# Kernel optimization log

Hardware: AMD Instinct MI355X
Metric: run time of the kernel (lower is better)

## Reference

```python
import jax, jax.numpy as jnp
import numpy as np

HID = 2048          # hidden_size
INTER = 4096        # expand * hidden_size
NH = 64             # num_heads
HD = 64             # head_dim (NH*HD == INTER)
N = 128             # ssm state_size
G = 1               # n_groups
K = 4               # conv_kernel
EPS = 1e-5
CONV_DIM = INTER + 2 * G * N            # 4352
PROJ = INTER + CONV_DIM + NH            # 8512 (d_mlp == 0)


def setup_inputs() -> dict:
    key = jax.random.key(0)
    ks = jax.random.split(key, 6)
    B, S = 2, 2048
    return {
        "hidden_states": jax.random.normal(ks[0], (B, S, HID), jnp.float32),
        "in_proj_w": jax.random.normal(ks[1], (PROJ, HID), jnp.float32) * 0.02,
        "conv_w": jax.random.normal(ks[2], (CONV_DIM, 1, K), jnp.float32) * 0.1,
        "conv_b": jax.random.normal(ks[3], (CONV_DIM,), jnp.float32) * 0.02,
        "dt_bias": jnp.ones((NH,), jnp.float32),
        "A_log": jnp.log(jnp.arange(1, NH + 1, dtype=jnp.float32)),
        "D": jnp.ones((NH,), jnp.float32),
        "norm_weight": jnp.ones((INTER,), jnp.float32),
        "out_proj_w": jax.random.normal(ks[4], (HID, INTER), jnp.float32) * 0.02,
    }


def _mamba2_forward(hidden_states, in_proj_w, conv_w, conv_b, dt_bias,
                    A_log, D, norm_weight, out_proj_w):
    b, sq, _ = hidden_states.shape
    # in_proj (d_mlp == 0, so split is gate | hidden_B_C | dt)
    proj = hidden_states @ in_proj_w.T                       # [b, s, PROJ]
    gate, hbc, dt = jnp.split(proj, [INTER, INTER + CONV_DIM], axis=-1)

    # causal depthwise conv1d over time + SiLU
    xc = jnp.transpose(hbc, (0, 2, 1))                       # [b, conv_dim, s]
    xc = jax.lax.conv_general_dilated(xc, conv_w, (1,), [(K - 1, 0)],
                                      feature_group_count=CONV_DIM)
    xc = xc + conv_b[None, :, None]
    hbc = jax.nn.silu(jnp.transpose(xc, (0, 2, 1)))          # [b, s, conv_dim]

    hs, Bm, Cm = jnp.split(hbc, [INTER, INTER + G * N], axis=-1)
    hs = hs.reshape(b, sq, NH, HD)
    Bm = jnp.repeat(Bm.reshape(b, sq, G, N), NH // G, axis=2)   # [b, s, nh, n]
    Cm = jnp.repeat(Cm.reshape(b, sq, G, N), NH // G, axis=2)

    A = -jnp.exp(A_log)                                      # [nh]
    dt = jax.nn.softplus(dt + dt_bias)                       # [b, s, nh]

    # selective SSM scan: state_t = exp(dt*A)*state_{t-1} + dt*B_t x_t^T
    def step(state, inp):
        xt, Bt, Ct, dtt = inp                                # [b,nh,hd],[b,nh,n],[b,nh,n],[b,nh]
        dA = jnp.exp(dtt * A)                                # [b, nh]
        state = state * dA[..., None, None] \
            + (dtt[..., None] * xt)[..., None] * Bt[:, :, None, :]
        y = jnp.einsum('bhdn,bhn->bhd', state, Ct)
        return state, y

    init = jnp.zeros((b, NH, HD, N), jnp.float32)
    xs = (jnp.moveaxis(hs, 1, 0), jnp.moveaxis(Bm, 1, 0),
          jnp.moveaxis(Cm, 1, 0), jnp.moveaxis(dt, 1, 0))
    _, ys = jax.lax.scan(step, init, xs)                     # [s, b, nh, hd]
    y = jnp.moveaxis(ys, 0, 1) + D[None, None, :, None] * hs
    y = y.reshape(b, sq, INTER)

    # gated RMSNorm (norm_before_gate=False): gate first, then normalize
    y = y * jax.nn.silu(gate)
    var = jnp.mean(y * y, axis=-1, keepdims=True)
    y = y * jax.lax.rsqrt(var + EPS) * norm_weight
    return y @ out_proj_w.T                                  # [b, s, HID]


def reference(hidden_states, in_proj_w, conv_w, conv_b, dt_bias, A_log, D,
              norm_weight, out_proj_w):
    return _mamba2_forward(hidden_states, in_proj_w, conv_w, conv_b, dt_bias,
                           A_log, D, norm_weight, out_proj_w)
```

## Files before the change

### kernel.cpp

```cpp
#include <hip/hip_runtime.h>
#include <hip/hip_bf16.h>
#include <cstddef>
#include <cstdint>

#define HID   2048
#define INTER 4096
#define NH    64
#define HD    64
#define NST   128
#define CONV_DIM 4352
#define PROJ  8512
#define PROJ_PAD 8704
#define SS    2048
#define BB    2
#define BS    (BB*SS)
#define EPS   1e-5f

#define COL_HS 4096
#define COL_B  8192
#define COL_C  8320
#define COL_DT 8448

#define NCHC  64
#define CHUNKC 32
#define CV8   (CONV_DIM / 8)

#define CL    128
#define NCHK  16

typedef short s16x8 __attribute__((ext_vector_type(8)));
typedef float f32x4 __attribute__((ext_vector_type(4)));

__device__ inline ushort f2b(float x) {
  __hip_bfloat16 h = __float2bfloat16(x);
  return *(ushort*)&h;
}
__device__ inline float b2f(ushort u) {
  unsigned int v = ((unsigned int)u) << 16;
  return __uint_as_float(v);
}
__device__ inline int swz(int row, int e) { return row * 128 + (e ^ ((row & 7) << 3)); }

__device__ inline void gload16(const void* g, void* l) {
  __builtin_amdgcn_global_load_lds((const __attribute__((address_space(1))) void*)g,
                                   (__attribute__((address_space(3))) void*)l, 16, 0, 0);
}

#define N4A  ((long)BS * HID / 4)
#define N4W1 ((long)PROJ_PAD * HID / 4)
#define N4W2 ((long)HID * INTER / 4)

__global__ __launch_bounds__(256) void convert_all(
    const float* __restrict__ hs, const float* __restrict__ w1,
    const float* __restrict__ w2, ushort* __restrict__ hs16,
    ushort* __restrict__ w1p, ushort* __restrict__ w216) {
  long i = (long)blockIdx.x * 256 + threadIdx.x;
  const float* src;
  ushort* dst;
  long e0;
  if (i < N4A) {
    src = hs; dst = hs16; e0 = i * 4;
  } else if (i < N4A + N4W1) {
    long k = i - N4A;
    e0 = k * 4;
    long row = e0 >> 11;
    if (row >= PROJ) {
      ushort4 z = {0, 0, 0, 0};
      *(ushort4*)(w1p + e0) = z;
      return;
    }
    src = w1; dst = w1p;
  } else if (i < N4A + N4W1 + N4W2) {
    long k = i - N4A - N4W1;
    src = w2; dst = w216; e0 = k * 4;
  } else {
    return;
  }
  float4 v = *(const float4*)(src + e0);
  ushort4 o;
  o.x = f2b(v.x); o.y = f2b(v.y); o.z = f2b(v.z); o.w = f2b(v.w);
  *(ushort4*)(dst + e0) = o;
}

__global__ __launch_bounds__(512, 2) void gemm256_8ph(
    const ushort* __restrict__ A, const ushort* __restrict__ Bw,
    ushort* __restrict__ C, float* __restrict__ dtbuf) {
  __shared__ ushort smem[65536];
  const int tid = threadIdx.x;
  const int lane = tid & 63;
  const int wid = tid >> 6;
  const int wm = wid >> 2;
  const int wn = wid & 3;
  const int r = lane & 15;
  const int kx = lane >> 4;

  const int fid = blockIdx.x;
  const int bcol = ((fid >> 7) << 3) + ((fid & 127) >> 4);
  const int brow = fid & 15;

  const ushort* Ag = A + (size_t)(brow * 256) * HID;
  const ushort* Bg = Bw + (size_t)(bcol * 256) * HID;

  const int srow = tid >> 3;
  const int scole = (((tid & 7) * 16) ^ ((srow & 7) << 4)) >> 1;

  auto stageA = [&](int buf, int kt, int half) {
    const ushort* g = Ag + (size_t)(half * 128 + srow) * HID + kt * 64 + scole;
    ushort* l = smem + buf * 16384 + half * 8192 + tid * 8;
    gload16(g, l);
    gload16(g + (size_t)64 * HID, l + 4096);
  };
  auto stageB = [&](int buf, int kt, int half) {
    const ushort* g = Bg + (size_t)(half * 128 + srow) * HID + kt * 64 + scole;
    ushort* l = smem + 32768 + buf * 16384 + half * 8192 + tid * 8;
    gload16(g, l);
    gload16(g + (size_t)64 * HID, l + 4096);
  };
  auto ldA = [&](int buf, int mf, int ks) -> s16x8 {
    int row = wm * 128 + mf * 16 + r;
    int cb = (ks * 64 + kx * 16) ^ ((row & 7) << 4);
    return *(const s16x8*)(smem + buf * 16384 + row * 64 + (cb >> 1));
  };
  auto ldB = [&](int buf, int nf, int ks) -> s16x8 {
    int row = wn * 64 + nf * 16 + r;
    int cb = (ks * 64 + kx * 16) ^ ((row & 7) << 4);
    return *(const s16x8*)(smem + 32768 + buf * 16384 + row * 64 + (cb >> 1));
  };

  f32x4 acc[8][4];
#pragma unroll
  for (int i = 0; i < 8; i++)
#pragma unroll
    for (int j = 0; j < 4; j++) acc[i][j] = (f32x4)0.f;

  constexpr int NT = HID / 64;

  stageA(0, 0, 0); stageA(0, 0, 1);
  stageB(0, 0, 0); stageB(0, 0, 1);
  stageA(1, 1, 0); stageA(1, 1, 1);
  asm volatile("s_waitcnt vmcnt(4)" ::: "memory");
  __builtin_amdgcn_s_barrier();

  int cur = 0;
  for (int t = 0; t < NT; t++) {
    s16x8 a[4][2], b[2][2], b2[2][2];
#pragma unroll
    for (int mf = 0; mf < 4; mf++)
#pragma unroll
      for (int ks = 0; ks < 2; ks++) a[mf][ks] = ldA(cur, mf, ks);
#pragma unroll
    for (int nf = 0; nf < 2; nf++)
#pragma unroll
      for (int ks = 0; ks < 2; ks++) b[nf][ks] = ldB(cur, nf, ks);
    if (t + 1 < NT) stageB(cur ^ 1, t + 1, 0);
    __builtin_amdgcn_s_barrier();
    asm volatile("s_waitcnt lgkmcnt(0)" ::: "memory");
    __builtin_amdgcn_sched_barrier(0);
    __builtin_amdgcn_s_setprio(1);
#pragma unroll
    for (int mf = 0; mf < 4; mf++)
#pragma unroll
      for (int nf = 0; nf < 2; nf++)
#pragma unroll
        for (int ks = 0; ks < 2; ks++)
          acc[mf][nf] = __builtin_amdgcn_mfma_f32_16x16x32_bf16(a[mf][ks], b[nf][ks], acc[mf][nf], 0, 0, 0);
    __builtin_amdgcn_s_setprio(0);
    __builtin_amdgcn_s_barrier();
#pragma unroll
    for (int nf = 0; nf < 2; nf++)
#pragma unroll
      for (int ks = 0; ks < 2; ks++) b2[nf][ks] = ldB(cur, nf + 2, ks);
    if (t + 1 < NT) stageB(cur ^ 1, t + 1, 1);
    __builtin_amdgcn_s_barrier();
    asm volatile("s_waitcnt lgkmcnt(0)" ::: "memory");
    __builtin_amdgcn_sched_barrier(0);
    __builtin_amdgcn_s_setprio(1);
#pragma unroll
    for (int mf = 0; mf < 4; mf++)
#pragma unroll
      for (int nf = 0; nf < 2; nf++)
#pragma unroll
        for (int ks = 0; ks < 2; ks++)
          acc[mf][nf + 2] = __builtin_amdgcn_mfma_f32_16x16x32_bf16(a[mf][ks], b2[nf][ks], acc[mf][nf + 2], 0, 0, 0);
    __builtin_amdgcn_s_setprio(0);
    __builtin_amdgcn_s_barrier();
#pragma unroll
    for (int mf = 0; mf < 4; mf++)
#pragma unroll
      for (int ks = 0; ks < 2; ks++) a[mf][ks] = ldA(cur, mf + 4, ks);
    __builtin_amdgcn_s_barrier();
    asm volatile("s_waitcnt lgkmcnt(0)" ::: "memory");
    __builtin_amdgcn_sched_barrier(0);
    __builtin_amdgcn_s_setprio(1);
#pragma unroll
    for (int mf = 0; mf < 4; mf++)
#pragma unroll
      for (int nf = 0; nf < 2; nf++)
#pragma unroll
        for (int ks = 0; ks < 2; ks++)
          acc[mf + 4][nf] = __builtin_amdgcn_mfma_f32_16x16x32_bf16(a[mf][ks], b[nf][ks], acc[mf + 4][nf], 0, 0, 0);
    __builtin_amdgcn_s_setprio(0);
    __builtin_amdgcn_s_barrier();
    if (t + 2 < NT) { stageA(cur, t + 2, 0); stageA(cur, t + 2, 1); }
    __builtin_amdgcn_s_setprio(1);
#pragma unroll
    for (int mf = 0; mf < 4; mf++)
#pragma unroll
      for (int nf = 0; nf < 2; nf++)
#pragma unroll
        for (int ks = 0; ks < 2; ks++)
          acc[mf + 4][nf + 2] = __builtin_amdgcn_mfma_f32_16x16x32_bf16(a[mf][ks], b2[nf][ks], acc[mf + 4][nf + 2], 0, 0, 0);
    __builtin_amdgcn_s_setprio(0);
    if (t + 2 < NT) {
      asm volatile("s_waitcnt vmcnt(4)" ::: "memory");
    } else {
      asm volatile("s_waitcnt vmcnt(0)" ::: "memory");
    }
    __builtin_amdgcn_s_barrier();
    cur ^= 1;
  }

  const int m0 = brow * 256 + wm * 128 + (lane >> 4) * 4;
  const int n0 = bcol * 256 + wn * 64 + r;
#pragma unroll
  for (int mf = 0; mf < 8; mf++) {
#pragma unroll
    for (int nf = 0; nf < 4; nf++) {
      int n = n0 + nf * 16;
      if (n >= PROJ) continue;
#pragma unroll
      for (int q = 0; q < 4; q++) {
        float v = acc[mf][nf][q];
        int m = m0 + mf * 16 + q;
        C[(size_t)m * PROJ + n] = f2b(v);
        if (n >= COL_DT) dtbuf[(size_t)m * 64 + (n - COL_DT)] = v;
      }
    }
  }
}

__global__ __launch_bounds__(512, 2) void gemm2_256x128(
    const ushort* __restrict__ A, const ushort* __restrict__ Bw,
    float* __restrict__ C) {
  __shared__ ushort smem[49152];
  const int tid = threadIdx.x;
  const int lane = tid & 63;
  const int wid = tid >> 6;
  const int wm = wid >> 1;
  const int wn = wid & 1;
  const int r = lane & 15;
  const int kx = lane >> 4;

  const int fid = blockIdx.x;
  const int bcol = fid >> 4;
  const int brow = fid & 15;

  const ushort* Ag = A + (size_t)(brow * 256) * PROJ;
  const ushort* Bg = Bw + (size_t)(bcol * 128) * INTER;

  const int srow = tid >> 3;
  const int scole = (((tid & 7) * 16) ^ ((srow & 7) << 4)) >> 1;

  auto stageA2 = [&](int buf, int kt) {
#pragma unroll
    for (int i = 0; i < 4; i++) {
      gload16(Ag + (size_t)(i * 64 + srow) * PROJ + kt * 64 + scole,
              smem + buf * 16384 + i * 4096 + tid * 8);
    }
  };
  auto stageB2 = [&](int buf, int kt) {
#pragma unroll
    for (int i = 0; i < 2; i++) {
      gload16(Bg + (size_t)(i * 64 + srow) * INTER + kt * 64 + scole,
              smem + 32768 + buf * 8192 + i * 4096 + tid * 8);
    }
  };
  auto ldA2 = [&](int buf, int mf, int ks) -> s16x8 {
    int row = wm * 64 + mf * 16 + r;
    int cb = (ks * 64 + kx * 16) ^ ((row & 7) << 4);
    return *(const s16x8*)(smem + buf * 16384 + row * 64 + (cb >> 1));
  };
  auto ldB2 = [&](int buf, int nf, int ks) -> s16x8 {
    int row = wn * 64 + nf * 16 + r;
    int cb = (ks * 64 + kx * 16) ^ ((row & 7) << 4);
    return *(const s16x8*)(smem + 32768 + buf * 8192 + row * 64 + (cb >> 1));
  };

  f32x4 acc[4][4];
#pragma unroll
  for (int i = 0; i < 4; i++)
#pragma unroll
    for (int j = 0; j < 4; j++) acc[i][j] = (f32x4)0.f;

  constexpr int NT = INTER / 64;

  stageA2(0, 0); stageB2(0, 0);
  stageA2(1, 1); stageB2(1, 1);
  asm volatile("s_waitcnt vmcnt(6)" ::: "memory");
  __builtin_amdgcn_s_barrier();

  int cur = 0;
  for (int t = 0; t < NT; t++) {
    s16x8 a[4][2], b[4][2];
#pragma unroll
    for (int mf = 0; mf < 4; mf++)
#pragma unroll
      for (int ks = 0; ks < 2; ks++) a[mf][ks] = ldA2(cur, mf, ks);
#pragma unroll
    for (int nf = 0; nf < 4; nf++)
#pragma unroll
      for (int ks = 0; ks < 2; ks++) b[nf][ks] = ldB2(cur, nf, ks);
    __builtin_amdgcn_s_barrier();
    asm volatile("s_waitcnt lgkmcnt(0)" ::: "memory");
    __builtin_amdgcn_sched_barrier(0);
    __builtin_amdgcn_s_setprio(1);
#pragma unroll
    for (int mf = 0; mf < 4; mf++)
#pragma unroll
      for (int nf = 0; nf < 2; nf++)
#pragma unroll
        for (int ks = 0; ks < 2; ks++)
          acc[mf][nf] = __builtin_amdgcn_mfma_f32_16x16x32_bf16(a[mf][ks], b[nf][ks], acc[mf][nf], 0, 0, 0);
    __builtin_amdgcn_s_setprio(0);
    __builtin_amdgcn_s_barrier();
    if (t + 2 < NT) { stageA2(cur, t + 2); stageB2(cur, t + 2); }
    __builtin_amdgcn_s_setprio(1);
#pragma unroll
    for (int mf = 0; mf < 4; mf++)
#pragma unroll
      for (int nf = 2; nf < 4; nf++)
#pragma unroll
        for (int ks = 0; ks < 2; ks++)
          acc[mf][nf] = __builtin_amdgcn_mfma_f32_16x16x32_bf16(a[mf][ks], b[nf][ks], acc[mf][nf], 0, 0, 0);
    __builtin_amdgcn_s_setprio(0);
    if (t + 2 < NT) {
      asm volatile("s_waitcnt vmcnt(6)" ::: "memory");
    } else {
      asm volatile("s_waitcnt vmcnt(0)" ::: "memory");
    }
    __builtin_amdgcn_s_barrier();
    cur ^= 1;
  }

  const int m0 = brow * 256 + wm * 64 + (lane >> 4) * 4;
  const int n0 = bcol * 128 + wn * 64 + r;
#pragma unroll
  for (int mf = 0; mf < 4; mf++) {
#pragma unroll
    for (int nf = 0; nf < 4; nf++) {
      int n = n0 + nf * 16;
#pragma unroll
      for (int q = 0; q < 4; q++)
        C[(size_t)(m0 + mf * 16 + q) * HID + n] = acc[mf][nf][q];
    }
  }
}

__global__ __launch_bounds__(256) void conv_capture(
    const ushort* __restrict__ proj, ushort* __restrict__ side) {
  int idx = blockIdx.x * 256 + threadIdx.x;
  const int total = BB * NCHC * 3 * CV8;
  if (idx >= total) return;
  int c8 = idx % CV8;
  int t = idx / CV8;
  int j = t % 3; t /= 3;
  int chunk = t % NCHC;
  int b = t / NCHC;
  int s = chunk * CHUNKC - 1 - j;
  s16x8 v = {0, 0, 0, 0, 0, 0, 0, 0};
  if (s >= 0) v = *(const s16x8*)(proj + ((size_t)b * SS + s) * PROJ + COL_HS + c8 * 8);
  *(s16x8*)(side + ((size_t)(b * NCHC + chunk) * 3 + j) * CONV_DIM + c8 * 8) = v;
}

__global__ __launch_bounds__(256) void conv_silu(
    ushort* __restrict__ proj, const ushort* __restrict__ side,
    const float* __restrict__ cw, const float* __restrict__ cb) {
  int idx = blockIdx.x * 256 + threadIdx.x;
  const int total = BB * NCHC * CV8;
  if (idx >= total) return;
  int c8 = idx % CV8;
  int t = idx / CV8;
  int chunk = t % NCHC;
  int b = t / NCHC;
  const int c0 = c8 * 8;
  float w0[8], w1[8], w2[8], w3[8], bias[8], h1[8], h2[8], h3[8];
#pragma unroll
  for (int e = 0; e < 8; e++) {
    float4 wv = *(const float4*)(cw + (c0 + e) * 4);
    w0[e] = wv.x; w1[e] = wv.y; w2[e] = wv.z; w3[e] = wv.w;
    bias[e] = cb[c0 + e];
  }
  const ushort* sd = side + (size_t)(b * NCHC + chunk) * 3 * CONV_DIM;
  {
    s16x8 v1 = *(const s16x8*)(sd + c0);
    s16x8 v2 = *(const s16x8*)(sd + CONV_DIM + c0);
    s16x8 v3 = *(const s16x8*)(sd + 2 * CONV_DIM + c0);
#pragma unroll
    for (int e = 0; e < 8; e++) {
      h1[e] = b2f((ushort)v1[e]);
      h2[e] = b2f((ushort)v2[e]);
      h3[e] = b2f((ushort)v3[e]);
    }
  }
  size_t p = ((size_t)b * SS + (size_t)chunk * CHUNKC) * PROJ + COL_HS + c0;
  for (int s = 0; s < CHUNKC; s++) {
    s16x8 xv = *(const s16x8*)(proj + p);
    s16x8 ov;
#pragma unroll
    for (int e = 0; e < 8; e++) {
      float x = b2f((ushort)xv[e]);
      float o = w3[e] * x + w2[e] * h1[e] + w1[e] * h2[e] + w0[e] * h3[e] + bias[e];
      o = o / (1.f + __expf(-o));
      ov[e] = (short)f2b(o);
      h3[e] = h2[e]; h2[e] = h1[e]; h1[e] = x;
    }
    *(s16x8*)(proj + p) = ov;
    p += PROJ;
  }
}

__global__ __launch_bounds__(256) void ssd_chunk_state(
    const ushort* __restrict__ proj, const float* __restrict__ dtf,
    const float* __restrict__ dt_bias, const float* __restrict__ A_log,
    ushort* __restrict__ states, float* __restrict__ cumbuf,
    float* __restrict__ dtvbuf) {
  const int bid = blockIdx.x;
  const int c = bid & 15;
  const int h = (bid >> 4) & 63;
  const int b = bid >> 10;
  const int tid = threadIdx.x;
  const int lane = tid & 63;
  const int wv = tid >> 6;
  __shared__ float sdtv[CL], scum[CL], sw[CL];
  __shared__ float wtot[2];
  __shared__ ushort sBt[128 * 128];
  __shared__ ushort sXw[64 * 128];
  const size_t row0 = (size_t)b * SS + (size_t)c * CL;
  const size_t bh = (size_t)(b * NH + h);

  const float Ah = -__expf(A_log[h]);
  float dtvv = 0.f, v = 0.f;
  if (tid < CL) {
    float z = dtf[(row0 + tid) * 64 + h] + dt_bias[h];
    dtvv = (z > 20.f) ? z : log1pf(__expf(z));
    v = dtvv * Ah;
  }
#pragma unroll
  for (int off = 1; off < 64; off <<= 1) {
    float u = __shfl_up(v, off);
    if (lane >= off) v += u;
  }
  if (tid < CL && lane == 63) wtot[wv] = v;
  __syncthreads();
  if (wv == 1) v += wtot[0];
  if (tid < CL) {
    sdtv[tid] = dtvv;
    scum[tid] = v;
    cumbuf[bh * SS + c * CL + tid] = v;
    dtvbuf[bh * SS + c * CL + tid] = dtvv;
  }
  __syncthreads();
  const float cumL = scum[CL - 1];
  if (tid < CL) sw[tid] = __expf(cumL - v) * dtvv;
  __syncthreads();

  {
    const int t = tid >> 1, n0 = (tid & 1) * 64;
    const ushort* src = proj + (row0 + t) * PROJ + COL_B + n0;
#pragma unroll
    for (int j = 0; j < 64; j += 8) {
      s16x8 vv = *(const s16x8*)(src + j);
#pragma unroll
      for (int e = 0; e < 8; e++) sBt[swz(n0 + j + e, t)] = (ushort)vv[e];
    }
  }
  {
    const int d = tid & 63;
    const int t0 = (tid >> 6) * 32;
    for (int t = t0; t < t0 + 32; t++) {
      float x = b2f(proj[(row0 + t) * PROJ + COL_HS + h * 64 + d]);
      sXw[swz(d, t)] = f2b(x * sw[t]);
    }
  }
  __syncthreads();

  const int r = lane & 15, kx = lane >> 4;
  f32x4 acc[2][4];
#pragma unroll
  for (int i = 0; i < 2; i++)
#pragma unroll
    for (int j = 0; j < 4; j++) acc[i][j] = (f32x4)0.f;
#pragma unroll
  for (int kk = 0; kk < 4; kk++) {
    s16x8 a[2], bo[4];
#pragma unroll
    for (int i = 0; i < 2; i++)
      a[i] = *(const s16x8*)&sBt[swz(wv * 32 + i * 16 + r, kk * 32 + kx * 8)];
#pragma unroll
    for (int j = 0; j < 4; j++)
      bo[j] = *(const s16x8*)&sXw[swz(j * 16 + r, kk * 32 + kx * 8)];
#pragma unroll
    for (int i = 0; i < 2; i++)
#pragma unroll
      for (int j = 0; j < 4; j++)
        acc[i][j] = __builtin_amdgcn_mfma_f32_16x16x32_bf16(a[i], bo[j], acc[i][j], 0, 0, 0);
  }
  ushort* dst = states + (size_t)bid * (128 * 64);
#pragma unroll
  for (int i = 0; i < 2; i++) {
#pragma unroll
    for (int j = 0; j < 4; j++) {
      int n = wv * 32 + i * 16 + (lane >> 4) * 4;
      int d = (lane & 15) + j * 16;
      ushort4 o;
      o.x = f2b(acc[i][j][0]);
      o.y = f2b(acc[i][j][1]);
      o.z = f2b(acc[i][j][2]);
      o.w = f2b(acc[i][j][3]);
      *(ushort4*)(dst + (size_t)d * 128 + n) = o;
    }
  }
}

__global__ __launch_bounds__(256) void ssd_state_scan(
    ushort* __restrict__ states, const float* __restrict__ cumbuf) {
  const int bh = blockIdx.x;
  const int tid = threadIdx.x;
  float run[32];
#pragma unroll
  for (int i = 0; i < 32; i++) run[i] = 0.f;
  for (int c = 0; c < NCHK; c++) {
    float dec = __expf(cumbuf[(size_t)bh * SS + c * CL + (CL - 1)]);
    ushort* p = states + ((size_t)bh * NCHK + c) * 8192 + tid * 32;
    s16x8 in[4];
#pragma unroll
    for (int v = 0; v < 4; v++) in[v] = *(const s16x8*)(p + v * 8);
    s16x8 out[4];
#pragma unroll
    for (int v = 0; v < 4; v++) {
#pragma unroll
      for (int e = 0; e < 8; e++) {
        int i = v * 8 + e;
        out[v][e] = (short)f2b(run[i]);
        run[i] = dec * run[i] + b2f((ushort)in[v][e]);
      }
    }
#pragma unroll
    for (int v = 0; v < 4; v++) *(s16x8*)(p + v * 8) = out[v];
  }
}

__global__ __launch_bounds__(256, 2) void ssd_chunk_out(
    ushort* __restrict__ proj, const ushort* __restrict__ states,
    const float* __restrict__ cumbuf, const float* __restrict__ dtvbuf,
    const float* __restrict__ Dp) {
  const int bid = blockIdx.x;
  const int c = bid & 15;
  const int h = (bid >> 4) & 63;
  const int b = bid >> 10;
  const int tid = threadIdx.x;
  const int lane = tid & 63;
  const int wv = tid >> 6;
  __shared__ ushort sB[128 * 128];
  __shared__ ushort sX[64 * 128];
  const size_t row0 = (size_t)b * SS + (size_t)c * CL;
  const size_t bh = (size_t)(b * NH + h);
  const float* cumb = cumbuf + bh * SS + c * CL;
  const float* dtvb = dtvbuf + bh * SS + c * CL;
  const int r = lane & 15, kx = lane >> 4;

  float ct[2][4];
#pragma unroll
  for (int i = 0; i < 2; i++)
#pragma unroll
    for (int q = 0; q < 4; q++)
      ct[i][q] = cumb[wv * 32 + i * 16 + ((lane >> 4) << 2) + q];
  float cumt[8], dvt[8];
#pragma unroll
  for (int j = 0; j < 8; j++) {
    int tau = j * 16 + (lane & 15);
    cumt[j] = cumb[tau];
    dvt[j] = dtvb[tau];
  }

  {
    const int t = tid >> 1, n0 = (tid & 1) * 64;
    const ushort* srcB = proj + (row0 + t) * PROJ + COL_B + n0;
#pragma unroll
    for (int j = 0; j < 64; j += 8)
      *(s16x8*)&sB[swz(t, n0 + j)] = *(const s16x8*)(srcB + j);
  }
  {
    const int d = tid & 63;
    const int t0 = (tid >> 6) * 32;
    for (int t = t0; t < t0 + 32; t++)
      sX[swz(d, t)] = proj[(row0 + t) * PROJ + COL_HS + h * 64 + d];
  }
  s16x8 cf[4][2];
#pragma unroll
  for (int kk = 0; kk < 4; kk++)
#pragma unroll
    for (int i = 0; i < 2; i++)
      cf[kk][i] = *(const s16x8*)(proj + (row0 + wv * 32 + i * 16 + r) * PROJ
                                  + COL_C + kk * 32 + kx * 8);
  __syncthreads();

  f32x4 g[2][8];
#pragma unroll
  for (int i = 0; i < 2; i++)
#pragma unroll
    for (int j = 0; j < 8; j++) g[i][j] = (f32x4)0.f;
#pragma unroll
  for (int kk = 0; kk < 4; kk++) {
    s16x8 bo[8];
#pragma unroll
    for (int j = 0; j < 8; j++)
      bo[j] = *(const s16x8*)&sB[swz(j * 16 + r, kk * 32 + kx * 8)];
#pragma unroll
    for (int i = 0; i < 2; i++)
#pragma unroll
      for (int j = 0; j < 8; j++)
        g[i][j] = __builtin_amdgcn_mfma_f32_16x16x32_bf16(cf[kk][i], bo[j], g[i][j], 0, 0, 0);
  }

  f32x4 yi[2][4];
#pragma unroll
  for (int i = 0; i < 2; i++)
#pragma unroll
    for (int j = 0; j < 4; j++) yi[i][j] = (f32x4)0.f;
  {
    const ushort* sp = states + (size_t)bid * 8192;
#pragma unroll
    for (int kk = 0; kk < 4; kk++) {
      s16x8 spk[4];
#pragma unroll
      for (int j = 0; j < 4; j++)
        spk[j] = *(const s16x8*)(sp + (size_t)(j * 16 + r) * 128 + kk * 32 + kx * 8);
#pragma unroll
      for (int i = 0; i < 2; i++)
#pragma unroll
        for (int j = 0; j < 4; j++)
          yi[i][j] = __builtin_amdgcn_mfma_f32_16x16x32_bf16(cf[kk][i], spk[j], yi[i][j], 0, 0, 0);
    }
  }
  __syncthreads();

#pragma unroll
  for (int j = 0; j < 8; j++) {
    float cu = cumt[j], dv = dvt[j];
    int tau = j * 16 + (lane & 15);
#pragma unroll
    for (int i = 0; i < 2; i++) {
#pragma unroll
      for (int q = 0; q < 4; q++) {
        int t = wv * 32 + i * 16 + ((lane >> 4) << 2) + q;
        float val = (tau <= t) ? g[i][j][q] * __expf(ct[i][q] - cu) * dv : 0.f;
        sB[swz(t, tau)] = f2b(val);
      }
    }
  }
  __syncthreads();

  f32x4 y[2][4];
#pragma unroll
  for (int i = 0; i < 2; i++)
#pragma unroll
    for (int j = 0; j < 4; j++) y[i][j] = (f32x4)0.f;
#pragma unroll
  for (int kk = 0; kk < 4; kk++) {
    s16x8 a[2], bo[4];
#pragma unroll
    for (int i = 0; i < 2; i++)
      a[i] = *(const s16x8*)&sB[swz(wv * 32 + i * 16 + r, kk * 32 + kx * 8)];
#pragma unroll
    for (int j = 0; j < 4; j++)
      bo[j] = *(const s16x8*)&sX[swz(j * 16 + r, kk * 32 + kx * 8)];
#pragma unroll
    for (int i = 0; i < 2; i++)
#pragma unroll
      for (int j = 0; j < 4; j++)
        y[i][j] = __builtin_amdgcn_mfma_f32_16x16x32_bf16(a[i], bo[j], y[i][j], 0, 0, 0);
  }

  const float Dh = Dp[h];
  float eP[2][4];
#pragma unroll
  for (int i = 0; i < 2; i++)
#pragma unroll
    for (int q = 0; q < 4; q++) eP[i][q] = __expf(ct[i][q]);
#pragma unroll
  for (int i = 0; i < 2; i++) {
#pragma unroll
    for (int j = 0; j < 4; j++) {
      int t0 = wv * 32 + i * 16 + (lane >> 4) * 4;
      int d = (lane & 15) + j * 16;
#pragma unroll
      for (int q = 0; q < 4; q++) {
        float x = b2f(sX[swz(d, t0 + q)]);
        proj[(row0 + t0 + q) * PROJ + COL_HS + h * 64 + d] =
            f2b(y[i][j][q] + eP[i][q] * yi[i][j][q] + Dh * x);
      }
    }
  }
}

__global__ __launch_bounds__(256) void rmsnorm_kernel(
    ushort* __restrict__ proj, const float* __restrict__ nw) {
  const int row = blockIdx.x;
  const int tid = threadIdx.x;
  ushort* yp = proj + (size_t)row * PROJ + COL_HS;
  const ushort* gp = proj + (size_t)row * PROJ;
  float v[16];
  float ss = 0.f;
#pragma unroll
  for (int q = 0; q < 4; q++) {
    int col = q * 1024 + tid * 4;
    ushort4 yv = *(const ushort4*)(yp + col);
    ushort4 gv = *(const ushort4*)(gp + col);
    float vy[4] = {b2f(yv.x), b2f(yv.y), b2f(yv.z), b2f(yv.w)};
    float vg[4] = {b2f(gv.x), b2f(gv.y), b2f(gv.z), b2f(gv.w)};
#pragma unroll
    for (int j = 0; j < 4; j++) {
      float sg = vg[j] / (1.f + __expf(-vg[j]));
      float vv = vy[j] * sg;
      v[q * 4 + j] = vv;
      ss += vv * vv;
    }
  }
#pragma unroll
  for (int o = 1; o < 64; o <<= 1) ss += __shfl_xor(ss, o);
  __shared__ float red[4];
  if ((tid & 63) == 0) red[tid >> 6] = ss;
  __syncthreads();
  float tot = red[0] + red[1] + red[2] + red[3];
  float scale = rsqrtf(tot * (1.f / INTER) + EPS);
#pragma unroll
  for (int q = 0; q < 4; q++) {
    int col = q * 1024 + tid * 4;
    float4 w = *(const float4*)(nw + col);
    ushort4 o;
    o.x = f2b(v[q * 4 + 0] * scale * w.x);
    o.y = f2b(v[q * 4 + 1] * scale * w.y);
    o.z = f2b(v[q * 4 + 2] * scale * w.z);
    o.w = f2b(v[q * 4 + 3] * scale * w.w);
    *(ushort4*)(yp + col) = o;
  }
}

extern "C" void kernel_launch(void* const* d_in, const int* in_sizes, int n_in,
                              void* d_out, int out_size, void* d_ws, size_t ws_size,
                              hipStream_t stream) {
  const float* hs   = (const float*)d_in[0];
  const float* w1   = (const float*)d_in[1];
  const float* cw   = (const float*)d_in[2];
  const float* cb   = (const float*)d_in[3];
  const float* dtb  = (const float*)d_in[4];
  const float* alog = (const float*)d_in[5];
  const float* Dp   = (const float*)d_in[6];
  const float* nw   = (const float*)d_in[7];
  const float* w2   = (const float*)d_in[8];
  float* out = (float*)d_out;

  char* base = (char*)d_ws;
  size_t off = 0;
  ushort* proj = (ushort*)(base + off); off += (size_t)BS * PROJ * 2;
  ushort* side = (ushort*)(base + off); off += (size_t)BB * NCHC * 3 * CONV_DIM * 2;
  off = (off + 255) & ~(size_t)255;
  float* dtbuf = (float*)(base + off); off += (size_t)BS * 64 * 4;
  off = (off + 255) & ~(size_t)255;
  ushort* w216 = (ushort*)(base + off); off += (size_t)HID * INTER * 2;
  off = (off + 255) & ~(size_t)255;
  char* rC = base + off;
  ushort* hs16 = (ushort*)rC;
  ushort* w1p  = (ushort*)(rC + 16777216);
  ushort* states = (ushort*)rC;
  float*  cumbuf = (float*)(rC + 33554432);
  float*  dtvbuf = (float*)(rC + 33554432 + 1048576);

  {
    long n4 = N4A + N4W1 + N4W2;
    convert_all<<<(int)((n4 + 255) / 256), 256, 0, stream>>>(hs, w1, w2, hs16, w1p, w216);
  }

  gemm256_8ph<<<(BS / 256) * (PROJ_PAD / 256), 512, 0, stream>>>(hs16, w1p, proj, dtbuf);

  conv_capture<<<(BB * NCHC * 3 * CV8 + 255) / 256, 256, 0, stream>>>(proj, side);
  conv_silu<<<(BB * NCHC * CV8 + 255) / 256, 256, 0, stream>>>(proj, side, cw, cb);

  ssd_chunk_state<<<BB * NH * NCHK, 256, 0, stream>>>(proj, dtbuf, dtb, alog, states, cumbuf, dtvbuf);
  ssd_state_scan<<<BB * NH, 256, 0, stream>>>(states, cumbuf);
  ssd_chunk_out<<<BB * NH * NCHK, 256, 0, stream>>>(proj, states, cumbuf, dtvbuf, Dp);

  rmsnorm_kernel<<<BS, 256, 0, stream>>>(proj, nw);

  gemm2_256x128<<<256, 512, 0, stream>>>(
      (const ushort*)(proj + COL_HS), w216, out);
}
```

Baseline: 430.7 us.

## Fuse conv capture and SiLU into out-of-place conv, split state scan across halves

Replaces the two-pass conv (capture chunk boundary rows into a side buffer, then an in-place sequential chunk conv) with one out-of-place kernel. Each thread handles 8 timesteps and reads its 3 previous rows directly from proj, writing into a compact xbc buffer. The SSD kernels now read x, B and C from that dense CONV_DIM-stride buffer. The state scan is also split across two blocks per (batch, head) for more parallelism. The cost is a new workspace buffer and re-reading 3 halo rows for every 8 outputs.

```diff
diff --git a/kernel.cpp b/kernel.cpp
--- a/kernel.cpp
+++ b/kernel.cpp
@@ -21,8 +21,9 @@
 #define COL_C  8320
 #define COL_DT 8448
 
-#define NCHC  64
-#define CHUNKC 32
+#define XBC_B  4096
+#define XBC_C  4224
+
 #define CV8   (CONV_DIM / 8)
 
 #define CL    128
@@ -356,33 +357,18 @@
   }
 }
 
-__global__ __launch_bounds__(256) void conv_capture(
-    const ushort* __restrict__ proj, ushort* __restrict__ side) {
+__global__ __launch_bounds__(256) void conv_fused(
+    const ushort* __restrict__ proj, ushort* __restrict__ xbc,
+    const float* __restrict__ cw, const float* __restrict__ cb) {
   int idx = blockIdx.x * 256 + threadIdx.x;
-  const int total = BB * NCHC * 3 * CV8;
+  const int total = BB * (SS / 8) * CV8;
   if (idx >= total) return;
   int c8 = idx % CV8;
   int t = idx / CV8;
-  int j = t % 3; t /= 3;
-  int chunk = t % NCHC;
-  int b = t / NCHC;
-  int s = chunk * CHUNKC - 1 - j;
-  s16x8 v = {0, 0, 0, 0, 0, 0, 0, 0};
-  if (s >= 0) v = *(const s16x8*)(proj + ((size_t)b * SS + s) * PROJ + COL_HS + c8 * 8);
-  *(s16x8*)(side + ((size_t)(b * NCHC + chunk) * 3 + j) * CONV_DIM + c8 * 8) = v;
-}
-
-__global__ __launch_bounds__(256) void conv_silu(
-    ushort* __restrict__ proj, const ushort* __restrict__ side,
-    const float* __restrict__ cw, const float* __restrict__ cb) {
-  int idx = blockIdx.x * 256 + threadIdx.x;
-  const int total = BB * NCHC * CV8;
-  if (idx >= total) return;
-  int c8 = idx % CV8;
-  int t = idx / CV8;
-  int chunk = t % NCHC;
-  int b = t / NCHC;
+  int s8 = t % (SS / 8);
+  int b = t / (SS / 8);
   const int c0 = c8 * 8;
+  const int s0 = s8 * 8;
   float w0[8], w1[8], w2[8], w3[8], bias[8], h1[8], h2[8], h3[8];
 #pragma unroll
   for (int e = 0; e < 8; e++) {
@@ -390,11 +376,12 @@
     w0[e] = wv.x; w1[e] = wv.y; w2[e] = wv.z; w3[e] = wv.w;
     bias[e] = cb[c0 + e];
   }
-  const ushort* sd = side + (size_t)(b * NCHC + chunk) * 3 * CONV_DIM;
+  const ushort* src = proj + ((size_t)b * SS + s0) * PROJ + COL_HS + c0;
   {
-    s16x8 v1 = *(const s16x8*)(sd + c0);
-    s16x8 v2 = *(const s16x8*)(sd + CONV_DIM + c0);
-    s16x8 v3 = *(const s16x8*)(sd + 2 * CONV_DIM + c0);
+    s16x8 v1 = {0,0,0,0,0,0,0,0}, v2 = v1, v3 = v1;
+    if (s0 >= 1) v1 = *(const s16x8*)(src - (size_t)1 * PROJ);
+    if (s0 >= 2) v2 = *(const s16x8*)(src - (size_t)2 * PROJ);
+    if (s0 >= 3) v3 = *(const s16x8*)(src - (size_t)3 * PROJ);
 #pragma unroll
     for (int e = 0; e < 8; e++) {
       h1[e] = b2f((ushort)v1[e]);
@@ -402,9 +389,10 @@
       h3[e] = b2f((ushort)v3[e]);
     }
   }
-  size_t p = ((size_t)b * SS + (size_t)chunk * CHUNKC) * PROJ + COL_HS + c0;
-  for (int s = 0; s < CHUNKC; s++) {
-    s16x8 xv = *(const s16x8*)(proj + p);
+  ushort* dst = xbc + ((size_t)b * SS + s0) * CONV_DIM + c0;
+#pragma unroll
+  for (int s = 0; s < 8; s++) {
+    s16x8 xv = *(const s16x8*)(src + (size_t)s * PROJ);
     s16x8 ov;
 #pragma unroll
     for (int e = 0; e < 8; e++) {
@@ -414,13 +402,12 @@
       ov[e] = (short)f2b(o);
       h3[e] = h2[e]; h2[e] = h1[e]; h1[e] = x;
     }
-    *(s16x8*)(proj + p) = ov;
-    p += PROJ;
+    *(s16x8*)(dst + (size_t)s * CONV_DIM) = ov;
   }
 }
 
 __global__ __launch_bounds__(256) void ssd_chunk_state(
-    const ushort* __restrict__ proj, const float* __restrict__ dtf,
+    const ushort* __restrict__ xbc, const float* __restrict__ dtf,
     const float* __restrict__ dt_bias, const float* __restrict__ A_log,
     ushort* __restrict__ states, float* __restrict__ cumbuf,
     float* __restrict__ dtvbuf) {
@@ -466,7 +453,7 @@
 
   {
     const int t = tid >> 1, n0 = (tid & 1) * 64;
-    const ushort* src = proj + (row0 + t) * PROJ + COL_B + n0;
+    const ushort* src = xbc + (row0 + t) * CONV_DIM + XBC_B + n0;
 #pragma unroll
     for (int j = 0; j < 64; j += 8) {
       s16x8 vv = *(const s16x8*)(src + j);
@@ -478,7 +465,7 @@
     const int d = tid & 63;
     const int t0 = (tid >> 6) * 32;
     for (int t = t0; t < t0 + 32; t++) {
-      float x = b2f(proj[(row0 + t) * PROJ + COL_HS + h * 64 + d]);
+      float x = b2f(xbc[(row0 + t) * CONV_DIM + h * 64 + d]);
       sXw[swz(d, t)] = f2b(x * sw[t]);
     }
   }
@@ -524,20 +511,21 @@
 
 __global__ __launch_bounds__(256) void ssd_state_scan(
     ushort* __restrict__ states, const float* __restrict__ cumbuf) {
-  const int bh = blockIdx.x;
+  const int bh = blockIdx.x >> 1;
+  const int half = blockIdx.x & 1;
   const int tid = threadIdx.x;
-  float run[32];
-#pragma unroll
-  for (int i = 0; i < 32; i++) run[i] = 0.f;
+  float run[16];
+#pragma unroll
+  for (int i = 0; i < 16; i++) run[i] = 0.f;
   for (int c = 0; c < NCHK; c++) {
     float dec = __expf(cumbuf[(size_t)bh * SS + c * CL + (CL - 1)]);
-    ushort* p = states + ((size_t)bh * NCHK + c) * 8192 + tid * 32;
-    s16x8 in[4];
-#pragma unroll
-    for (int v = 0; v < 4; v++) in[v] = *(const s16x8*)(p + v * 8);
-    s16x8 out[4];
-#pragma unroll
-    for (int v = 0; v < 4; v++) {
+    ushort* p = states + ((size_t)bh * NCHK + c) * 8192 + half * 4096 + tid * 16;
+    s16x8 in[2];
+#pragma unroll
+    for (int v = 0; v < 2; v++) in[v] = *(const s16x8*)(p + v * 8);
+    s16x8 out[2];
+#pragma unroll
+    for (int v = 0; v < 2; v++) {
 #pragma unroll
       for (int e = 0; e < 8; e++) {
         int i = v * 8 + e;
@@ -546,14 +534,14 @@
       }
     }
 #pragma unroll
-    for (int v = 0; v < 4; v++) *(s16x8*)(p + v * 8) = out[v];
+    for (int v = 0; v < 2; v++) *(s16x8*)(p + v * 8) = out[v];
   }
 }
 
 __global__ __launch_bounds__(256, 2) void ssd_chunk_out(
-    ushort* __restrict__ proj, const ushort* __restrict__ states,
-    const float* __restrict__ cumbuf, const float* __restrict__ dtvbuf,
-    const float* __restrict__ Dp) {
+    ushort* __restrict__ proj, const ushort* __restrict__ xbc,
+    const ushort* __restrict__ states, const float* __restrict__ cumbuf,
+    const float* __restrict__ dtvbuf, const float* __restrict__ Dp) {
   const int bid = blockIdx.x;
   const int c = bid & 15;
   const int h = (bid >> 4) & 63;
@@ -585,7 +573,7 @@
 
   {
     const int t = tid >> 1, n0 = (tid & 1) * 64;
-    const ushort* srcB = proj + (row0 + t) * PROJ + COL_B + n0;
+    const ushort* srcB = xbc + (row0 + t) * CONV_DIM + XBC_B + n0;
 #pragma unroll
     for (int j = 0; j < 64; j += 8)
       *(s16x8*)&sB[swz(t, n0 + j)] = *(const s16x8*)(srcB + j);
@@ -594,15 +582,15 @@
     const int d = tid & 63;
     const int t0 = (tid >> 6) * 32;
     for (int t = t0; t < t0 + 32; t++)
-      sX[swz(d, t)] = proj[(row0 + t) * PROJ + COL_HS + h * 64 + d];
+      sX[swz(d, t)] = xbc[(row0 + t) * CONV_DIM + h * 64 + d];
   }
   s16x8 cf[4][2];
 #pragma unroll
   for (int kk = 0; kk < 4; kk++)
 #pragma unroll
     for (int i = 0; i < 2; i++)
-      cf[kk][i] = *(const s16x8*)(proj + (row0 + wv * 32 + i * 16 + r) * PROJ
-                                  + COL_C + kk * 32 + kx * 8);
+      cf[kk][i] = *(const s16x8*)(xbc + (row0 + wv * 32 + i * 16 + r) * CONV_DIM
+                                  + XBC_C + kk * 32 + kx * 8);
   __syncthreads();
 
   f32x4 g[2][8];
@@ -764,7 +752,8 @@
   char* base = (char*)d_ws;
   size_t off = 0;
   ushort* proj = (ushort*)(base + off); off += (size_t)BS * PROJ * 2;
-  ushort* side = (ushort*)(base + off); off += (size_t)BB * NCHC * 3 * CONV_DIM * 2;
+  off = (off + 255) & ~(size_t)255;
+  ushort* xbc = (ushort*)(base + off); off += (size_t)BS * CONV_DIM * 2;
   off = (off + 255) & ~(size_t)255;
   float* dtbuf = (float*)(base + off); off += (size_t)BS * 64 * 4;
   off = (off + 255) & ~(size_t)255;
@@ -784,12 +773,11 @@
 
   gemm256_8ph<<<(BS / 256) * (PROJ_PAD / 256), 512, 0, stream>>>(hs16, w1p, proj, dtbuf);
 
-  conv_capture<<<(BB * NCHC * 3 * CV8 + 255) / 256, 256, 0, stream>>>(proj, side);
-  conv_silu<<<(BB * NCHC * CV8 + 255) / 256, 256, 0, stream>>>(proj, side, cw, cb);
-
-  ssd_chunk_state<<<BB * NH * NCHK, 256, 0, stream>>>(proj, dtbuf, dtb, alog, states, cumbuf, dtvbuf);
-  ssd_state_scan<<<BB * NH, 256, 0, stream>>>(states, cumbuf);
-  ssd_chunk_out<<<BB * NH * NCHK, 256, 0, stream>>>(proj, states, cumbuf, dtvbuf, Dp);
+  conv_fused<<<(BB * (SS / 8) * CV8 + 255) / 256, 256, 0, stream>>>(proj, xbc, cw, cb);
+
+  ssd_chunk_state<<<BB * NH * NCHK, 256, 0, stream>>>(xbc, dtbuf, dtb, alog, states, cumbuf, dtvbuf);
+  ssd_state_scan<<<BB * NH * 2, 256, 0, stream>>>(states, cumbuf);
+  ssd_chunk_out<<<BB * NH * NCHK, 256, 0, stream>>>(proj, xbc, states, cumbuf, dtvbuf, Dp);
 
   rmsnorm_kernel<<<BS, 256, 0, stream>>>(proj, nw);
 
```

After: 405.1 us. 1.06x faster.
